# Optimization experiments

Hardware: AMD Instinct MI355X
Metric: run time of the kernel (lower is better)

Reference implementation:

```python
import jax, jax.numpy as jnp
import numpy as np

B, S, H = 16, 4096, 768
NUM_WORDS = S // 2  # 2048: max distinct words per sample (padded output width)


def setup_inputs() -> dict:
    key = jax.random.key(0)
    k1, k2 = jax.random.split(key)
    hidden_states = jax.random.normal(k1, (B, S, H), dtype=jnp.float32)
    # word ids: non-decreasing, contiguous from 0; -1 marks special tokens (None in HF)
    inc = jax.random.bernoulli(k2, 0.5, (B, S)).astype(jnp.int32)
    inc = inc.at[:, :2].set(0)  # keep word 0 alive at position 1 after masking CLS
    word_ids = jnp.maximum(jnp.cumsum(inc, axis=1) - 1, 0)
    word_ids = jnp.minimum(word_ids, NUM_WORDS - 1)  # static cap on segment count
    word_ids = word_ids.at[:, 0].set(-1)   # [CLS]
    word_ids = word_ids.at[:, -1].set(-1)  # [SEP]
    return {"hidden_states": hidden_states, "word_ids": word_ids}


def reference(hidden_states, word_ids):
    # Segment-mean of subword embeddings into word embeddings.
    # hidden_states: [B, S, H] float; word_ids: [B, S] int, -1 = special token (dropped).
    b, s, h = hidden_states.shape
    valid = word_ids >= 0  # [B, S]
    # offset per-sample word ids into a flat segment space of size B*NUM_WORDS;
    # invalid tokens go to segment (b*NUM_WORDS + 0) but contribute zeros.
    wid = jnp.where(valid, word_ids, 0)
    seg = (wid + jnp.arange(b, dtype=word_ids.dtype)[:, None] * NUM_WORDS).reshape(-1)
    data = jnp.where(valid[..., None], hidden_states, 0.0).reshape(b * s, h)
    sums = jax.ops.segment_sum(data, seg, num_segments=b * NUM_WORDS)
    counts = jax.ops.segment_sum(
        valid.reshape(-1).astype(hidden_states.dtype), seg, num_segments=b * NUM_WORDS
    )
    sums = sums.reshape(b, NUM_WORDS, h)
    counts = counts.reshape(b, NUM_WORDS)
    # mean per word; words with zero tokens stay 0 (matches pad_sequence zero-padding)
    return sums / jnp.maximum(counts, 1.0)[..., None]
```

## Files before the change

### kernel.cpp

```cpp
#include <hip/hip_runtime.h>

constexpr int B = 16;
constexpr int S = 4096;
constexpr int H = 768;
constexpr int NW = 2048;
constexpr int V4 = H / 4;
constexpr int WPW = 8;
constexpr int WAVES_PER_BLK = 4;
constexpr int GPS = NW / WPW;

__global__ __launch_bounds__(256)
void find_starts_kernel(const int* __restrict__ wid, int* __restrict__ starts) {
    const int idx = blockIdx.x * 256 + threadIdx.x;
    const int s = idx & (S - 1);
    const int b = idx >> 12;
    if (s < 1 || s >= S - 1) return;
    const int* __restrict__ row = wid + (size_t)b * S;
    const int cur = row[s];
    if (cur != row[s - 1] && cur >= 0) starts[b * NW + cur] = s;
}

__device__ __forceinline__ void acc4(float4& a, const float4 v) {
    a.x += v.x; a.y += v.y; a.z += v.z; a.w += v.w;
}

__global__ __launch_bounds__(64 * WAVES_PER_BLK)
void seg_mean_kernel(const float* __restrict__ hs,
                     const int* __restrict__ wid,
                     const int* __restrict__ starts,
                     float* __restrict__ out) {
    const int wave = threadIdx.x >> 6;
    const int lane = threadIdx.x & 63;
    const int gw = blockIdx.x * WAVES_PER_BLK + wave;
    const int b = gw >> 8;
    const int w0 = (gw & (GPS - 1)) * WPW;
    const int base_blk = b * NW + w0;

    int ctrl;
    if (lane <= WPW) {
        const int i = base_blk + lane;
        ctrl = (i < B * NW) ? starts[i] : (S - 1);
    } else if (lane == WPW + 1) {
        ctrl = wid[(size_t)b * S + (S - 2)];
    } else {
        ctrl = 0;
    }
    const int maxw = __builtin_amdgcn_readlane(ctrl, WPW + 1);

    const float4* __restrict__ base = (const float4*)(hs + (size_t)b * S * H);
    float4* __restrict__ obase = (float4*)(out + (size_t)base_blk * H);

#pragma unroll
    for (int i = 0; i < WPW; ++i) {
        const int w = w0 + i;
        const int start = __builtin_amdgcn_readlane(ctrl, i);
        int end = (w == maxw) ? (S - 1) : __builtin_amdgcn_readlane(ctrl, i + 1);
        if (w > maxw) end = start;

        float4 a0 = make_float4(0.f, 0.f, 0.f, 0.f), a1 = a0, a2 = a0;
        int s = start;
        for (; s + 1 < end; s += 2) {
            const float4* p0 = base + (size_t)s * V4;
            const float4* p1 = p0 + V4;
            float4 v0 = p0[lane], v1 = p0[lane + 64], v2 = p0[lane + 128];
            float4 u0 = p1[lane], u1 = p1[lane + 64], u2 = p1[lane + 128];
            acc4(a0, v0); acc4(a1, v1); acc4(a2, v2);
            acc4(a0, u0); acc4(a1, u1); acc4(a2, u2);
        }
        if (s < end) {
            const float4* p0 = base + (size_t)s * V4;
            float4 v0 = p0[lane], v1 = p0[lane + 64], v2 = p0[lane + 128];
            acc4(a0, v0); acc4(a1, v1); acc4(a2, v2);
        }

        const int cnt = end - start;
        const float inv = 1.0f / (float)(cnt > 0 ? cnt : 1);
        a0.x *= inv; a0.y *= inv; a0.z *= inv; a0.w *= inv;
        a1.x *= inv; a1.y *= inv; a1.z *= inv; a1.w *= inv;
        a2.x *= inv; a2.y *= inv; a2.z *= inv; a2.w *= inv;

        float4* __restrict__ o = obase + (size_t)i * V4;
        o[lane] = a0; o[lane + 64] = a1; o[lane + 128] = a2;
    }
}

extern "C" void kernel_launch(void* const* d_in, const int* in_sizes, int n_in,
                              void* d_out, int out_size, void* d_ws, size_t ws_size,
                              hipStream_t stream) {
    const float* hs = (const float*)d_in[0];
    const int* wid = (const int*)d_in[1];
    float* out = (float*)d_out;
    int* starts = (int*)d_ws;

    find_starts_kernel<<<(B * S) / 256, 256, 0, stream>>>(wid, starts);
    seg_mean_kernel<<<(B * GPS) / WAVES_PER_BLK, 64 * WAVES_PER_BLK, 0, stream>>>(
        hs, wid, starts, out);
}
```

Before: 334.2 us.

## Software-pipeline token loads across word boundaries with a D-deep register ring

```diff
diff --git a/kernel.cpp b/kernel.cpp
--- a/kernel.cpp
+++ b/kernel.cpp
@@ -8,6 +8,7 @@
 constexpr int WPW = 8;
 constexpr int WAVES_PER_BLK = 4;
 constexpr int GPS = NW / WPW;
+constexpr int D = 6;
 
 __global__ __launch_bounds__(256)
 void find_starts_kernel(const int* __restrict__ wid, int* __restrict__ starts) {
@@ -24,7 +25,7 @@
     a.x += v.x; a.y += v.y; a.z += v.z; a.w += v.w;
 }
 
-__global__ __launch_bounds__(64 * WAVES_PER_BLK)
+__global__ __launch_bounds__(64 * WAVES_PER_BLK, 4)
 void seg_mean_kernel(const float* __restrict__ hs,
                      const int* __restrict__ wid,
                      const int* __restrict__ starts,
@@ -47,40 +48,75 @@
     }
     const int maxw = __builtin_amdgcn_readlane(ctrl, WPW + 1);
 
+    float4* __restrict__ obase = (float4*)(out + (size_t)base_blk * H);
+    const float4 z = make_float4(0.f, 0.f, 0.f, 0.f);
+
+    if (w0 > maxw) {
+#pragma unroll
+        for (int i = 0; i < WPW; ++i) {
+            float4* o = obase + (size_t)i * V4;
+            o[lane] = z; o[lane + 64] = z; o[lane + 128] = z;
+        }
+        return;
+    }
+
+    const int nw_exist = min(WPW, maxw - w0 + 1);
+    const int last_w = w0 + nw_exist - 1;
+    const int s_begin = __builtin_amdgcn_readlane(ctrl, 0);
+    const int s_end = (last_w == maxw)
+                          ? (S - 1)
+                          : __builtin_amdgcn_readlane(ctrl, nw_exist);
+
     const float4* __restrict__ base = (const float4*)(hs + (size_t)b * S * H);
-    float4* __restrict__ obase = (float4*)(out + (size_t)base_blk * H);
 
+    float4 r0[D], r1[D], r2[D];
 #pragma unroll
-    for (int i = 0; i < WPW; ++i) {
-        const int w = w0 + i;
-        const int start = __builtin_amdgcn_readlane(ctrl, i);
-        int end = (w == maxw) ? (S - 1) : __builtin_amdgcn_readlane(ctrl, i + 1);
-        if (w > maxw) end = start;
+    for (int j = 0; j < D; ++j) {
+        int t = s_begin + j;
+        t = (t < s_end) ? t : (s_end - 1);
+        const float4* p = base + (size_t)t * V4;
+        r0[j] = p[lane]; r1[j] = p[lane + 64]; r2[j] = p[lane + 128];
+    }
 
-        float4 a0 = make_float4(0.f, 0.f, 0.f, 0.f), a1 = a0, a2 = a0;
-        int s = start;
-        for (; s + 1 < end; s += 2) {
-            const float4* p0 = base + (size_t)s * V4;
-            const float4* p1 = p0 + V4;
-            float4 v0 = p0[lane], v1 = p0[lane + 64], v2 = p0[lane + 128];
-            float4 u0 = p1[lane], u1 = p1[lane + 64], u2 = p1[lane + 128];
-            acc4(a0, v0); acc4(a1, v1); acc4(a2, v2);
-            acc4(a0, u0); acc4(a1, u1); acc4(a2, u2);
+    int widx = 0;
+    int cur_start = s_begin;
+    int cur_end = (w0 == maxw) ? (S - 1) : __builtin_amdgcn_readlane(ctrl, 1);
+    float4 a0 = z, a1 = z, a2 = z;
+    int t = s_begin;
+    int tload = s_begin + D;
+
+    while (t < s_end) {
+#pragma unroll
+        for (int j = 0; j < D; ++j) {
+            if (t < s_end) {
+                acc4(a0, r0[j]); acc4(a1, r1[j]); acc4(a2, r2[j]);
+                int tl = (tload < s_end) ? tload : (s_end - 1);
+                const float4* p = base + (size_t)tl * V4;
+                r0[j] = p[lane]; r1[j] = p[lane + 64]; r2[j] = p[lane + 128];
+                ++tload;
+                ++t;
+                if (t == cur_end) {
+                    const float inv = 1.0f / (float)(cur_end - cur_start);
+                    float4 m0 = a0, m1 = a1, m2 = a2;
+                    m0.x *= inv; m0.y *= inv; m0.z *= inv; m0.w *= inv;
+                    m1.x *= inv; m1.y *= inv; m1.z *= inv; m1.w *= inv;
+                    m2.x *= inv; m2.y *= inv; m2.z *= inv; m2.w *= inv;
+                    float4* o = obase + (size_t)widx * V4;
+                    o[lane] = m0; o[lane + 64] = m1; o[lane + 128] = m2;
+                    a0 = z; a1 = z; a2 = z;
+                    ++widx;
+                    cur_start = cur_end;
+                    const int w = w0 + widx;
+                    cur_end = (w >= maxw) ? (S - 1)
+                                          : __builtin_amdgcn_readlane(ctrl, widx + 1);
+                }
+            }
         }
-        if (s < end) {
-            const float4* p0 = base + (size_t)s * V4;
-            float4 v0 = p0[lane], v1 = p0[lane + 64], v2 = p0[lane + 128];
-            acc4(a0, v0); acc4(a1, v1); acc4(a2, v2);
-        }
+    }
 
-        const int cnt = end - start;
-        const float inv = 1.0f / (float)(cnt > 0 ? cnt : 1);
-        a0.x *= inv; a0.y *= inv; a0.z *= inv; a0.w *= inv;
-        a1.x *= inv; a1.y *= inv; a1.z *= inv; a1.w *= inv;
-        a2.x *= inv; a2.y *= inv; a2.z *= inv; a2.w *= inv;
-
-        float4* __restrict__ o = obase + (size_t)i * V4;
-        o[lane] = a0; o[lane + 64] = a1; o[lane + 128] = a2;
+    for (int i = nw_exist; i < WPW; ++i) {
+        float4* o = obase + (size_t)i * V4;
+        o[lane] = z; o[lane + 64] = z; o[lane + 128] = z;
     }
 }
 
```

Measured after the change: 358.6 us. 7.3% more time.

## Fuse segment-start detection into token-window segment-mean kernel

Applied to the files above, without the earlier changes.

```diff
diff --git a/kernel.cpp b/kernel.cpp
--- a/kernel.cpp
+++ b/kernel.cpp
@@ -5,82 +5,127 @@
 constexpr int H = 768;
 constexpr int NW = 2048;
 constexpr int V4 = H / 4;
-constexpr int WPW = 8;
+constexpr int W = 8;
+constexpr int WPS = 512;
 constexpr int WAVES_PER_BLK = 4;
-constexpr int GPS = NW / WPW;
-
-__global__ __launch_bounds__(256)
-void find_starts_kernel(const int* __restrict__ wid, int* __restrict__ starts) {
-    const int idx = blockIdx.x * 256 + threadIdx.x;
-    const int s = idx & (S - 1);
-    const int b = idx >> 12;
-    if (s < 1 || s >= S - 1) return;
-    const int* __restrict__ row = wid + (size_t)b * S;
-    const int cur = row[s];
-    if (cur != row[s - 1] && cur >= 0) starts[b * NW + cur] = s;
-}
 
 __device__ __forceinline__ void acc4(float4& a, const float4 v) {
     a.x += v.x; a.y += v.y; a.z += v.z; a.w += v.w;
 }
 
-__global__ __launch_bounds__(64 * WAVES_PER_BLK)
+__global__ __launch_bounds__(256)
 void seg_mean_kernel(const float* __restrict__ hs,
                      const int* __restrict__ wid,
-                     const int* __restrict__ starts,
                      float* __restrict__ out) {
     const int wave = threadIdx.x >> 6;
     const int lane = threadIdx.x & 63;
-    const int gw = blockIdx.x * WAVES_PER_BLK + wave;
-    const int b = gw >> 8;
-    const int w0 = (gw & (GPS - 1)) * WPW;
-    const int base_blk = b * NW + w0;
+    const int gwin = blockIdx.x * WAVES_PER_BLK + wave;
+    const int b = gwin >> 9;
+    const int win = gwin & (WPS - 1);
+    const int t0 = 1 + win * W;
 
-    int ctrl;
-    if (lane <= WPW) {
-        const int i = base_blk + lane;
-        ctrl = (i < B * NW) ? starts[i] : (S - 1);
-    } else if (lane == WPW + 1) {
-        ctrl = wid[(size_t)b * S + (S - 2)];
-    } else {
-        ctrl = 0;
-    }
-    const int maxw = __builtin_amdgcn_readlane(ctrl, WPW + 1);
+    const int* __restrict__ wrow = wid + (size_t)b * S;
+
+    int gidx = t0 - 1 + lane;
+    if (gidx > S - 1) gidx = S - 1;
+    if (lane == 63) gidx = S - 2;
+    const int wv = wrow[gidx];
 
     const float4* __restrict__ base = (const float4*)(hs + (size_t)b * S * H);
-    float4* __restrict__ obase = (float4*)(out + (size_t)base_blk * H);
+#define TOKS(X) X(0) X(1) X(2) X(3) X(4) X(5) X(6) X(7)
+#define DECL(J) float4 rA##J, rB##J, rC##J;
+    TOKS(DECL)
+#define LOADTOK(J) { int t = t0 + J; if (t > S - 2) t = S - 2;              \
+        const float4* p = base + (size_t)t * V4;                           \
+        rA##J = p[lane]; rB##J = p[lane + 64]; rC##J = p[lane + 128]; }
+    TOKS(LOADTOK)
+    __builtin_amdgcn_sched_barrier(0);
 
-#pragma unroll
-    for (int i = 0; i < WPW; ++i) {
-        const int w = w0 + i;
-        const int start = __builtin_amdgcn_readlane(ctrl, i);
-        int end = (w == maxw) ? (S - 1) : __builtin_amdgcn_readlane(ctrl, i + 1);
-        if (w > maxw) end = start;
+    const int maxw = __builtin_amdgcn_readlane(wv, 63);
 
-        float4 a0 = make_float4(0.f, 0.f, 0.f, 0.f), a1 = a0, a2 = a0;
-        int s = start;
-        for (; s + 1 < end; s += 2) {
-            const float4* p0 = base + (size_t)s * V4;
+    const int wprev = __shfl_up(wv, 1);
+    const bool chg = (lane >= 1) && (lane <= 62) && (wv != wprev);
+    const unsigned long long mask = __ballot(chg);
+
+    const float4 z = make_float4(0.f, 0.f, 0.f, 0.f);
+    float4 a0 = z, a1 = z, a2 = z;
+    int cnt = 0, wcur = 0;
+    bool active = false;
+
+    auto flush = [&]() {
+        const float inv = 1.0f / (float)cnt;
+        float4 m0 = a0, m1 = a1, m2 = a2;
+        m0.x *= inv; m0.y *= inv; m0.z *= inv; m0.w *= inv;
+        m1.x *= inv; m1.y *= inv; m1.z *= inv; m1.w *= inv;
+        m2.x *= inv; m2.y *= inv; m2.z *= inv; m2.w *= inv;
+        float4* o = (float4*)(out + ((size_t)b * NW + wcur) * H);
+        o[lane] = m0; o[lane + 64] = m1; o[lane + 128] = m2;
+    };
+
+#define STEP(J) {                                                          \
+        if ((mask >> (J + 1)) & 1ull) {                                    \
+            if (active) flush();                                           \
+            const int wval = __builtin_amdgcn_readlane(wv, J + 1);         \
+            active = (wval >= 0);                                          \
+            if (active) { wcur = wval; a0 = z; a1 = z; a2 = z; cnt = 0; }  \
+        }                                                                  \
+        if (active) { acc4(a0, rA##J); acc4(a1, rB##J); acc4(a2, rC##J); ++cnt; } }
+    TOKS(STEP)
+#undef STEP
+#undef LOADTOK
+#undef DECL
+#undef TOKS
+
+    if (active) {
+        int end;
+        const unsigned long long hi = mask >> 9;
+        if (hi) {
+            end = t0 + 8 + __builtin_ctzll(hi);
+        } else {
+            end = t0 + 62;
+            while (true) {
+                int t = end + lane;
+                if (t > S - 1) t = S - 1;
+                const int wv2 = wrow[t];
+                const unsigned long long m2 = __ballot(wv2 != wcur);
+                if (m2) { end += __builtin_ctzll(m2); break; }
+                end += 64;
+            }
+        }
+        cnt += end - (t0 + 8);
+        int t = t0 + 8;
+        for (; t + 3 < end; t += 4) {
+            const float4* p0 = base + (size_t)t * V4;
             const float4* p1 = p0 + V4;
-            float4 v0 = p0[lane], v1 = p0[lane + 64], v2 = p0[lane + 128];
-            float4 u0 = p1[lane], u1 = p1[lane + 64], u2 = p1[lane + 128];
-            acc4(a0, v0); acc4(a1, v1); acc4(a2, v2);
-            acc4(a0, u0); acc4(a1, u1); acc4(a2, u2);
+            const float4* p2 = p1 + V4;
+            const float4* p3 = p2 + V4;
+            float4 x00 = p0[lane], x01 = p0[lane + 64], x02 = p0[lane + 128];
+            float4 x10 = p1[lane], x11 = p1[lane + 64], x12 = p1[lane + 128];
+            float4 x20 = p2[lane], x21 = p2[lane + 64], x22 = p2[lane + 128];
+            float4 x30 = p3[lane], x31 = p3[lane + 64], x32 = p3[lane + 128];
+            acc4(a0, x00); acc4(a1, x01); acc4(a2, x02);
+            acc4(a0, x10); acc4(a1, x11); acc4(a2, x12);
+            acc4(a0, x20); acc4(a1, x21); acc4(a2, x22);
+            acc4(a0, x30); acc4(a1, x31); acc4(a2, x32);
         }
-        if (s < end) {
-            const float4* p0 = base + (size_t)s * V4;
-            float4 v0 = p0[lane], v1 = p0[lane + 64], v2 = p0[lane + 128];
+        for (; t < end; ++t) {
+            const float4* p = base + (size_t)t * V4;
+            float4 v0 = p[lane], v1 = p[lane + 64], v2 = p[lane + 128];
             acc4(a0, v0); acc4(a1, v1); acc4(a2, v2);
         }
+        flush();
+    }
 
-        const int cnt = end - start;
-        const float inv = 1.0f / (float)(cnt > 0 ? cnt : 1);
-        a0.x *= inv; a0.y *= inv; a0.z *= inv; a0.w *= inv;
-        a1.x *= inv; a1.y *= inv; a1.z *= inv; a1.w *= inv;
-        a2.x *= inv; a2.y *= inv; a2.z *= inv; a2.w *= inv;
-
-        float4* __restrict__ o = obase + (size_t)i * V4;
-        o[lane] = a0; o[lane + 64] = a1; o[lane + 128] = a2;
+    {
+        const int wz0 = win * 4;
+#pragma unroll
+        for (int k = 0; k < 4; ++k) {
+            const int w = wz0 + k;
+            if (w > maxw) {
+                float4* o = (float4*)(out + ((size_t)b * NW + w) * H);
+                o[lane] = z; o[lane + 64] = z; o[lane + 128] = z;
+            }
+        }
     }
 }
 
@@ -90,9 +135,7 @@
     const float* hs = (const float*)d_in[0];
     const int* wid = (const int*)d_in[1];
     float* out = (float*)d_out;
-    int* starts = (int*)d_ws;
 
-    find_starts_kernel<<<(B * S) / 256, 256, 0, stream>>>(wid, starts);
-    seg_mean_kernel<<<(B * GPS) / WAVES_PER_BLK, 64 * WAVES_PER_BLK, 0, stream>>>(
-        hs, wid, starts, out);
+    seg_mean_kernel<<<(B * WPS) / WAVES_PER_BLK, 64 * WAVES_PER_BLK, 0, stream>>>(
+        hs, wid, out);
 }
```

Measured after the change: 309.8 us. 1.08x faster.
